# Kernel optimization log

Hardware: AMD Instinct MI355X
Metric: run time of the kernel (lower is better)

Reference implementation:

```python
import jax, jax.numpy as jnp
import numpy as np
from jax import lax

SINKHORN_ITERS = 20


def sinkhorn_knopp(logits, tau=1.0, iterations=SINKHORN_ITERS):
    # logits: [N, K]. Log-domain alternating row/col normalization.
    N, K = logits.shape
    P = logits / tau
    log_target_col_sum = jnp.log(jnp.asarray(N / K, dtype=logits.dtype) + 1e-9)

    def step(P, _):
        P = P - jax.nn.logsumexp(P, axis=1, keepdims=True)   # row sums -> 1
        P = P - jax.nn.logsumexp(P, axis=0, keepdims=True) + log_target_col_sum  # col sums -> N/K
        return P, None

    P, _ = lax.scan(step, P, None, length=iterations)
    return jnp.exp(P)


def setup_inputs() -> dict:
    key = jax.random.key(0)
    ks = jax.random.split(key, 8)
    N, C, K, B = 200000, 128, 32, 16
    x = jax.random.normal(ks[0], (N, C), dtype=jnp.float32)
    batch = jnp.sort(jax.random.randint(ks[1], (N,), 0, B))
    # assign_mlp: Linear(C,C) -> ReLU -> Linear(C,K)
    W1 = jax.random.normal(ks[2], (C, C), dtype=jnp.float32) / np.sqrt(C)
    b1 = jnp.zeros((C,), dtype=jnp.float32)
    W2 = jax.random.normal(ks[3], (C, K), dtype=jnp.float32) / np.sqrt(C)
    b2 = jnp.zeros((K,), dtype=jnp.float32)
    scaling = jnp.asarray(5.0, dtype=jnp.float32)
    return {"x": x, "batch": batch, "W1": W1, "b1": b1, "W2": W2, "b2": b2,
            "scaling": scaling, "num_graphs": B}


def reference(x, batch, W1, b1, W2, b2, scaling, num_graphs):
    # assignment logits: MLP(x) * scaling  -> [N, K]
    h = jax.nn.relu(x @ W1 + b1)
    logits = (h @ W2 + b2) * scaling
    # doubly-stochastic soft assignment via Sinkhorn-Knopp (tau=1.0, 20 iters)
    s = sinkhorn_knopp(logits, tau=1.0, iterations=SINKHORN_ITERS)  # [N, K]
    # pooled super-node features: scatter-sum over graphs of s[n,k]*x[n,c]
    onehot = jax.nn.one_hot(batch, num_graphs, dtype=x.dtype)        # [N, B]
    out = jnp.einsum('nb,nk,nc->bkc', onehot, s, x)                  # [B, K, C]
    return out
```

## Files before the change

### kernel.cpp

```cpp
#include <hip/hip_runtime.h>
#include <hip/hip_bf16.h>

#define C_DIM 128
#define K_DIM 32
#define N_ITERS 20
#define NSHARD 16
#define WPAD 136
#define SK_THREADS 832
#define SK_WAVES 13

typedef __attribute__((ext_vector_type(8))) short short8;
typedef __attribute__((ext_vector_type(4))) float f32x4;
typedef __attribute__((ext_vector_type(4))) unsigned short us4;

__device__ __forceinline__ unsigned short f2bf(float f) {
    __hip_bfloat16 h = __float2bfloat16(f);
    return *reinterpret_cast<unsigned short*>(&h);
}

__global__ void init_kernel(float* __restrict__ out, int n_out,
                            float* __restrict__ zreg, int n_z,
                            const float* __restrict__ W1, const float* __restrict__ W2,
                            unsigned short* __restrict__ W1t,
                            unsigned short* __restrict__ W2t) {
    int i = blockIdx.x * blockDim.x + threadIdx.x;
    int stride = gridDim.x * blockDim.x;
    for (int j = i; j < n_out; j += stride) out[j] = 0.f;
    for (int j = i; j < n_z; j += stride) zreg[j] = 0.f;
    for (int j = i; j < C_DIM * C_DIM; j += stride) {
        int n = j >> 7, k = j & 127;
        W1t[j] = f2bf(W1[k * C_DIM + n]);
    }
    for (int j = i; j < C_DIM * K_DIM; j += stride) {
        int n = j >> 7, k = j & 127;
        W2t[j] = f2bf(W2[k * K_DIM + n]);
    }
}

__global__ __launch_bounds__(256, 4) void mlp_kernel(
    const float* __restrict__ x, const unsigned short* __restrict__ W1t,
    const float* __restrict__ b1, const unsigned short* __restrict__ W2t,
    const float* __restrict__ b2, const float* __restrict__ scal,
    float* __restrict__ Lg, int N, int ntiles) {
    __shared__ unsigned short sW1[C_DIM][WPAD];
    __shared__ unsigned short sW2[K_DIM][WPAD];
    __shared__ unsigned short sX[64][WPAD];
    __shared__ unsigned short sH[4][16][WPAD];
    __shared__ float sB1[C_DIM];
    __shared__ float sB2[K_DIM];

    const int tid = threadIdx.x;
    for (int i = tid; i < C_DIM * 16; i += 256) {
        const int r = i >> 4, c8 = (i & 15) * 8;
        *(float4*)&sW1[r][c8] = *(const float4*)&W1t[r * C_DIM + c8];
    }
    for (int i = tid; i < K_DIM * 16; i += 256) {
        const int r = i >> 4, c8 = (i & 15) * 8;
        *(float4*)&sW2[r][c8] = *(const float4*)&W2t[r * C_DIM + c8];
    }
    if (tid < C_DIM) sB1[tid] = b1[tid];
    if (tid < K_DIM) sB2[tid] = b2[tid];
    const float sc = *scal;

    const int wave = tid >> 6;
    const int lane = tid & 63;
    const int lr = lane & 15;
    const int kg = lane >> 4;
    __syncthreads();

    for (int tile = blockIdx.x; tile < ntiles; tile += gridDim.x) {
        const int row0 = tile * 64;
        __syncthreads();
        for (int i = tid; i < 2048; i += 256) {
            const int r = i >> 5, c4 = (i & 31) * 4;
            const float4 v = *(const float4*)&x[(size_t)(row0 + r) * C_DIM + c4];
            us4 u;
            u.x = f2bf(v.x); u.y = f2bf(v.y); u.z = f2bf(v.z); u.w = f2bf(v.w);
            *(us4*)&sX[r][c4] = u;
        }
        __syncthreads();

        short8 a[4];
#pragma unroll
        for (int kt = 0; kt < 4; ++kt)
            a[kt] = *(const short8*)&sX[wave * 16 + lr][kt * 32 + kg * 8];
#pragma unroll
        for (int ct = 0; ct < 8; ++ct) {
            const float bv = sB1[ct * 16 + lr];
            f32x4 acc = {bv, bv, bv, bv};
#pragma unroll
            for (int kt = 0; kt < 4; ++kt) {
                const short8 b = *(const short8*)&sW1[ct * 16 + lr][kt * 32 + kg * 8];
                acc = __builtin_amdgcn_mfma_f32_16x16x32_bf16(a[kt], b, acc, 0, 0, 0);
            }
#pragma unroll
            for (int r = 0; r < 4; ++r)
                sH[wave][kg * 4 + r][ct * 16 + lr] = f2bf(fmaxf(acc[r], 0.f));
        }
        __syncthreads();

        short8 a2[4];
#pragma unroll
        for (int kt = 0; kt < 4; ++kt)
            a2[kt] = *(const short8*)&sH[wave][lr][kt * 32 + kg * 8];
#pragma unroll
        for (int ct = 0; ct < 2; ++ct) {
            const float bv = sB2[ct * 16 + lr];
            f32x4 acc = {bv, bv, bv, bv};
#pragma unroll
            for (int kt = 0; kt < 4; ++kt) {
                const short8 b = *(const short8*)&sW2[ct * 16 + lr][kt * 32 + kg * 8];
                acc = __builtin_amdgcn_mfma_f32_16x16x32_bf16(a2[kt], b, acc, 0, 0, 0);
            }
#pragma unroll
            for (int r = 0; r < 4; ++r) {
                const int g = row0 + wave * 16 + kg * 4 + r;
                Lg[(size_t)g * K_DIM + ct * 16 + lr] = acc[r] * sc;
            }
        }
    }
}

__device__ __forceinline__ int bitrev5(int l) {
    return ((l & 1) << 4) | ((l & 2) << 2) | (l & 4) | ((l & 8) >> 2) |
           ((l & 16) >> 4);
}

#define FOLD_STAGE(M, HALF)                                   \
    {                                                         \
        const bool hi = (lane & (M)) != 0;                    \
        _Pragma("unroll")                                     \
        for (int j = 0; j < (HALF); ++j) {                    \
            const float give = hi ? p[j] : p[j + (HALF)];     \
            const float keep = hi ? p[j + (HALF)] : p[j];     \
            p[j] = keep + __shfl_xor(give, (M));              \
        }                                                     \
    }

__global__ __launch_bounds__(SK_THREADS) void sinkhorn_kernel(
    float* __restrict__ Lg, float* __restrict__ shards,
    float* __restrict__ vglob, int* __restrict__ arrive, int* __restrict__ done,
    int N, int nblocks) {
    __shared__ float sv[K_DIM];
    __shared__ float swsum[SK_WAVES][K_DIM];
    __shared__ float sdl[K_DIM];
    __shared__ int is_last;
    const int tid = threadIdx.x;
    const int wave = tid >> 6;
    const int lane = tid & 63;
    const size_t n = (size_t)blockIdx.x * SK_THREADS + tid;
    const bool valid = n < (size_t)N;
    const int myshard = blockIdx.x & (NSHARD - 1);
    const float log_tgt = __logf((float)N / (float)K_DIM);

    if (tid < K_DIM) sv[tid] = 0.f;

    float L[K_DIM];
    if (valid) {
        const float4* Lr = (const float4*)(Lg + n * K_DIM);
#pragma unroll
        for (int j = 0; j < 8; ++j) {
            const float4 v = Lr[j];
            L[4 * j] = v.x; L[4 * j + 1] = v.y; L[4 * j + 2] = v.z; L[4 * j + 3] = v.w;
        }
    } else {
#pragma unroll
        for (int j = 0; j < K_DIM; ++j) L[j] = 0.f;
    }
    __syncthreads();

    float m0 = 0.f, inv = 0.f;
    for (int t = 1; t <= N_ITERS; ++t) {
        float p[K_DIM];
        if (valid) {
#pragma unroll
            for (int j = 0; j < K_DIM; ++j) p[j] = L[j] - sv[j];
            m0 = p[0];
#pragma unroll
            for (int j = 1; j < K_DIM; ++j) m0 = fmaxf(m0, p[j]);
            float sum = 0.f;
#pragma unroll
            for (int j = 0; j < K_DIM; ++j) {
                p[j] = __expf(p[j] - m0);
                sum += p[j];
            }
            inv = 1.f / sum;
#pragma unroll
            for (int j = 0; j < K_DIM; ++j) p[j] *= inv;
        } else {
#pragma unroll
            for (int j = 0; j < K_DIM; ++j) p[j] = 0.f;
        }

        FOLD_STAGE(1, 16)
        FOLD_STAGE(2, 8)
        FOLD_STAGE(4, 4)
        FOLD_STAGE(8, 2)
        FOLD_STAGE(16, 1)
        const float tot = p[0] + __shfl_xor(p[0], 32);
        if (lane < K_DIM) swsum[wave][bitrev5(lane)] = tot;
        __syncthreads();
        if (tid < K_DIM) {
            float s_ = 0.f;
#pragma unroll
            for (int w = 0; w < SK_WAVES; ++w) s_ += swsum[w][tid];
            atomicAdd(&shards[((size_t)t * NSHARD + myshard) * K_DIM + tid], s_);
        }
        asm volatile("s_waitcnt vmcnt(0)" ::: "memory");
        __syncthreads();
        if (tid == 0) {
            const int old = __hip_atomic_fetch_add(arrive + t, 1, __ATOMIC_RELAXED,
                                                   __HIP_MEMORY_SCOPE_AGENT);
            is_last = (old == nblocks - 1);
        }
        __syncthreads();
        if (is_last) {
            if (tid < K_DIM) {
                float cs = 0.f;
#pragma unroll
                for (int sh = 0; sh < NSHARD; ++sh)
                    cs += __hip_atomic_load(
                        &shards[((size_t)t * NSHARD + sh) * K_DIM + tid],
                        __ATOMIC_RELAXED, __HIP_MEMORY_SCOPE_AGENT);
                const float v = (t < N_ITERS) ? (__logf(cs) - log_tgt)
                                              : ((float)N / (float)K_DIM) / cs;
                __hip_atomic_store(&vglob[t * K_DIM + tid], v, __ATOMIC_RELAXED,
                                   __HIP_MEMORY_SCOPE_AGENT);
            }
            asm volatile("s_waitcnt vmcnt(0)" ::: "memory");
            __syncthreads();
            if (tid == 0)
                __hip_atomic_store(done + t, 1, __ATOMIC_RELAXED,
                                   __HIP_MEMORY_SCOPE_AGENT);
        } else {
            if (tid == 0) {
                while (__hip_atomic_load(done + t, __ATOMIC_RELAXED,
                                         __HIP_MEMORY_SCOPE_AGENT) == 0)
                    __builtin_amdgcn_s_sleep(2);
            }
        }
        __syncthreads();
        if (tid < K_DIM) {
            const float v = __hip_atomic_load(&vglob[t * K_DIM + tid],
                                              __ATOMIC_RELAXED,
                                              __HIP_MEMORY_SCOPE_AGENT);
            if (t < N_ITERS) sv[tid] += v;
            else sdl[tid] = v;
        }
        __syncthreads();
    }

    if (valid) {
        float4* Sr = (float4*)(Lg + n * K_DIM);
#pragma unroll
        for (int j = 0; j < 8; ++j) {
            float4 o;
            o.x = __expf(L[4 * j + 0] - sv[4 * j + 0] - m0) * inv * sdl[4 * j + 0];
            o.y = __expf(L[4 * j + 1] - sv[4 * j + 1] - m0) * inv * sdl[4 * j + 1];
            o.z = __expf(L[4 * j + 2] - sv[4 * j + 2] - m0) * inv * sdl[4 * j + 2];
            o.w = __expf(L[4 * j + 3] - sv[4 * j + 3] - m0) * inv * sdl[4 * j + 3];
            Sr[j] = o;
        }
    }
}

#define PCHUNK 96
#define PCH_PER_BLOCK 4

__global__ __launch_bounds__(256) void pool_kernel(
    const float* __restrict__ x, const int* __restrict__ batch,
    const float* __restrict__ Sg, float* __restrict__ out, int N) {
    __shared__ float sx[PCHUNK][C_DIM];
    __shared__ float ss[PCHUNK][K_DIM];
    __shared__ int sb[PCHUNK];

    const int tid = threadIdx.x;
    const int k0 = (tid >> 5) * 4;
    const int c0 = (tid & 31) * 4;
    float acc[4][4];
#pragma unroll
    for (int i = 0; i < 4; ++i)
#pragma unroll
        for (int j = 0; j < 4; ++j) acc[i][j] = 0.f;

    int cur_b = -1;
    const int base0 = blockIdx.x * (PCHUNK * PCH_PER_BLOCK);

    for (int cc = 0; cc < PCH_PER_BLOCK; ++cc) {
        const int base = base0 + cc * PCHUNK;
        if (base >= N) break;
        const int rows = min(PCHUNK, N - base);
        __syncthreads();
        {
            const float4* src = (const float4*)(x + (size_t)base * C_DIM);
            for (int i = tid; i < rows * (C_DIM / 4); i += 256)
                ((float4*)&sx[0][0])[i] = src[i];
            const float4* ssrc = (const float4*)(Sg + (size_t)base * K_DIM);
            for (int i = tid; i < rows * (K_DIM / 4); i += 256)
                ((float4*)&ss[0][0])[i] = ssrc[i];
        }
        if (tid < rows) sb[tid] = batch[base + tid];
        __syncthreads();

        for (int r = 0; r < rows; ++r) {
            const int b = sb[r];
            if (b != cur_b) {
                if (cur_b >= 0) {
                    float* ob = out + ((size_t)cur_b * K_DIM + k0) * C_DIM + c0;
#pragma unroll
                    for (int i = 0; i < 4; ++i)
#pragma unroll
                        for (int j = 0; j < 4; ++j) {
                            atomicAdd(&ob[i * C_DIM + j], acc[i][j]);
                            acc[i][j] = 0.f;
                        }
                }
                cur_b = b;
            }
            const float4 sv = *(const float4*)&ss[r][k0];
            const float4 xv = *(const float4*)&sx[r][c0];
            const float sA[4] = {sv.x, sv.y, sv.z, sv.w};
            const float xA[4] = {xv.x, xv.y, xv.z, xv.w};
#pragma unroll
            for (int i = 0; i < 4; ++i)
#pragma unroll
                for (int j = 0; j < 4; ++j)
                    acc[i][j] = fmaf(sA[i], xA[j], acc[i][j]);
        }
    }
    if (cur_b >= 0) {
        float* ob = out + ((size_t)cur_b * K_DIM + k0) * C_DIM + c0;
#pragma unroll
        for (int i = 0; i < 4; ++i)
#pragma unroll
            for (int j = 0; j < 4; ++j) atomicAdd(&ob[i * C_DIM + j], acc[i][j]);
    }
}

extern "C" void kernel_launch(void* const* d_in, const int* in_sizes, int n_in,
                              void* d_out, int out_size, void* d_ws, size_t ws_size,
                              hipStream_t stream) {
    const float* x = (const float*)d_in[0];
    const int* batch = (const int*)d_in[1];
    const float* W1 = (const float*)d_in[2];
    const float* b1 = (const float*)d_in[3];
    const float* W2 = (const float*)d_in[4];
    const float* b2 = (const float*)d_in[5];
    const float* scal = (const float*)d_in[6];
    float* out = (float*)d_out;

    const int N = in_sizes[1];

    float* Lg = (float*)d_ws;
    float* shards = Lg + (size_t)N * K_DIM;
    const int n_shard_f = (N_ITERS + 1) * NSHARD * K_DIM;
    int* arrive = (int*)(shards + n_shard_f);
    int* done = arrive + 32;
    float* vglob = (float*)(done + 32);
    const int n_vglob = (N_ITERS + 1) * K_DIM;
    unsigned short* W1t = (unsigned short*)(vglob + n_vglob);
    unsigned short* W2t = W1t + C_DIM * C_DIM;
    const int n_z = n_shard_f + 64 + n_vglob;

    init_kernel<<<64, 256, 0, stream>>>(out, out_size, shards, n_z,
                                        W1, W2, W1t, W2t);

    const int ntiles = N / 64;
    mlp_kernel<<<640, 256, 0, stream>>>(x, W1t, b1, W2t, b2, scal, Lg, N, ntiles);

    const int sblocks = 256;
    sinkhorn_kernel<<<sblocks, SK_THREADS, 0, stream>>>(Lg, shards, vglob,
                                                        arrive, done, N, sblocks);

    const int pblocks = (N + PCHUNK * PCH_PER_BLOCK - 1) / (PCHUNK * PCH_PER_BLOCK);
    pool_kernel<<<pblocks, 256, 0, stream>>>(x, batch, Lg, out, N);
}
```

Before: 491.1 us.

## Precompute exp of logits and use hierarchical grid barrier in Sinkhorn

The Sinkhorn loop is rewritten in the multiplicative domain. Each row's exp(L - max) is computed once, so every iteration reduces to a dot product with per-column scale factors and one reciprocal, replacing 32 exps per row per iteration. The single-level grid barrier, where all blocks atomically arrive on one counter and spin on one flag, becomes a two-level tree: 16 groups of 16 blocks, with group leaders signalling followers. This should cut both ALU work and barrier contention, but it adds more flags and spin paths, and the multiplicative form can overflow or underflow when column scales grow large.

```diff
diff --git a/kernel.cpp b/kernel.cpp
--- a/kernel.cpp
+++ b/kernel.cpp
@@ -4,10 +4,11 @@
 #define C_DIM 128
 #define K_DIM 32
 #define N_ITERS 20
-#define NSHARD 16
 #define WPAD 136
 #define SK_THREADS 832
 #define SK_WAVES 13
+#define NGRP 16
+#define GSIZE 16
 
 typedef __attribute__((ext_vector_type(8))) short short8;
 typedef __attribute__((ext_vector_type(4))) float f32x4;
@@ -138,59 +139,53 @@
     }
 
 __global__ __launch_bounds__(SK_THREADS) void sinkhorn_kernel(
-    float* __restrict__ Lg, float* __restrict__ shards,
-    float* __restrict__ vglob, int* __restrict__ arrive, int* __restrict__ done,
-    int N, int nblocks) {
+    float* __restrict__ Lg, float* __restrict__ shards, float* __restrict__ vglob,
+    int* __restrict__ garr, int* __restrict__ rarr, int* __restrict__ done,
+    int* __restrict__ gdone, int N) {
     __shared__ float sv[K_DIM];
+    __shared__ float sw[K_DIM];
+    __shared__ float swsd[K_DIM];
     __shared__ float swsum[SK_WAVES][K_DIM];
-    __shared__ float sdl[K_DIM];
-    __shared__ int is_last;
     const int tid = threadIdx.x;
     const int wave = tid >> 6;
     const int lane = tid & 63;
+    const int g = blockIdx.x >> 4;
     const size_t n = (size_t)blockIdx.x * SK_THREADS + tid;
     const bool valid = n < (size_t)N;
-    const int myshard = blockIdx.x & (NSHARD - 1);
     const float log_tgt = __logf((float)N / (float)K_DIM);
 
-    if (tid < K_DIM) sv[tid] = 0.f;
-
-    float L[K_DIM];
+    if (tid < K_DIM) { sv[tid] = 0.f; sw[tid] = 1.f; }
+
+    float E[K_DIM];
     if (valid) {
         const float4* Lr = (const float4*)(Lg + n * K_DIM);
 #pragma unroll
         for (int j = 0; j < 8; ++j) {
             const float4 v = Lr[j];
-            L[4 * j] = v.x; L[4 * j + 1] = v.y; L[4 * j + 2] = v.z; L[4 * j + 3] = v.w;
-        }
+            E[4 * j] = v.x; E[4 * j + 1] = v.y; E[4 * j + 2] = v.z; E[4 * j + 3] = v.w;
+        }
+        float M = E[0];
+#pragma unroll
+        for (int j = 1; j < K_DIM; ++j) M = fmaxf(M, E[j]);
+#pragma unroll
+        for (int j = 0; j < K_DIM; ++j) E[j] = __expf(E[j] - M);
     } else {
 #pragma unroll
-        for (int j = 0; j < K_DIM; ++j) L[j] = 0.f;
+        for (int j = 0; j < K_DIM; ++j) E[j] = 0.f;
     }
     __syncthreads();
 
-    float m0 = 0.f, inv = 0.f;
+    float r_last = 0.f;
     for (int t = 1; t <= N_ITERS; ++t) {
+        float up = 0.f;
+#pragma unroll
+        for (int j = 0; j < K_DIM; ++j) up = fmaf(E[j], sw[j], up);
+        float r = 0.f;
+        if (valid) r = 1.0f / up;
+        r_last = r;
         float p[K_DIM];
-        if (valid) {
-#pragma unroll
-            for (int j = 0; j < K_DIM; ++j) p[j] = L[j] - sv[j];
-            m0 = p[0];
-#pragma unroll
-            for (int j = 1; j < K_DIM; ++j) m0 = fmaxf(m0, p[j]);
-            float sum = 0.f;
-#pragma unroll
-            for (int j = 0; j < K_DIM; ++j) {
-                p[j] = __expf(p[j] - m0);
-                sum += p[j];
-            }
-            inv = 1.f / sum;
-#pragma unroll
-            for (int j = 0; j < K_DIM; ++j) p[j] *= inv;
-        } else {
-#pragma unroll
-            for (int j = 0; j < K_DIM; ++j) p[j] = 0.f;
-        }
+#pragma unroll
+        for (int j = 0; j < K_DIM; ++j) p[j] = E[j] * r;
 
         FOLD_STAGE(1, 16)
         FOLD_STAGE(2, 8)
@@ -200,52 +195,77 @@
         const float tot = p[0] + __shfl_xor(p[0], 32);
         if (lane < K_DIM) swsum[wave][bitrev5(lane)] = tot;
         __syncthreads();
-        if (tid < K_DIM) {
-            float s_ = 0.f;
-#pragma unroll
-            for (int w = 0; w < SK_WAVES; ++w) s_ += swsum[w][tid];
-            atomicAdd(&shards[((size_t)t * NSHARD + myshard) * K_DIM + tid], s_);
-        }
-        asm volatile("s_waitcnt vmcnt(0)" ::: "memory");
-        __syncthreads();
-        if (tid == 0) {
-            const int old = __hip_atomic_fetch_add(arrive + t, 1, __ATOMIC_RELAXED,
-                                                   __HIP_MEMORY_SCOPE_AGENT);
-            is_last = (old == nblocks - 1);
-        }
-        __syncthreads();
-        if (is_last) {
-            if (tid < K_DIM) {
-                float cs = 0.f;
-#pragma unroll
-                for (int sh = 0; sh < NSHARD; ++sh)
-                    cs += __hip_atomic_load(
-                        &shards[((size_t)t * NSHARD + sh) * K_DIM + tid],
-                        __ATOMIC_RELAXED, __HIP_MEMORY_SCOPE_AGENT);
-                const float v = (t < N_ITERS) ? (__logf(cs) - log_tgt)
-                                              : ((float)N / (float)K_DIM) / cs;
-                __hip_atomic_store(&vglob[t * K_DIM + tid], v, __ATOMIC_RELAXED,
-                                   __HIP_MEMORY_SCOPE_AGENT);
+
+        if (wave == 0) {
+            if (lane < K_DIM) {
+                float s_ = 0.f;
+#pragma unroll
+                for (int w = 0; w < SK_WAVES; ++w) s_ += swsum[w][lane];
+                atomicAdd(&shards[((size_t)t * NGRP + g) * K_DIM + lane], s_);
             }
             asm volatile("s_waitcnt vmcnt(0)" ::: "memory");
-            __syncthreads();
-            if (tid == 0)
-                __hip_atomic_store(done + t, 1, __ATOMIC_RELAXED,
-                                   __HIP_MEMORY_SCOPE_AGENT);
-        } else {
-            if (tid == 0) {
-                while (__hip_atomic_load(done + t, __ATOMIC_RELAXED,
-                                         __HIP_MEMORY_SCOPE_AGENT) == 0)
-                    __builtin_amdgcn_s_sleep(2);
-            }
-        }
-        __syncthreads();
-        if (tid < K_DIM) {
-            const float v = __hip_atomic_load(&vglob[t * K_DIM + tid],
-                                              __ATOMIC_RELAXED,
-                                              __HIP_MEMORY_SCOPE_AGENT);
-            if (t < N_ITERS) sv[tid] += v;
-            else sdl[tid] = v;
+            int is_gl = 0, is_rl = 0;
+            if (lane == 0) {
+                const int ga = __hip_atomic_fetch_add(&garr[t * NGRP + g], 1,
+                                                      __ATOMIC_RELAXED,
+                                                      __HIP_MEMORY_SCOPE_AGENT);
+                is_gl = (ga == GSIZE - 1);
+                if (is_gl) {
+                    const int ra = __hip_atomic_fetch_add(&rarr[t], 1,
+                                                          __ATOMIC_RELAXED,
+                                                          __HIP_MEMORY_SCOPE_AGENT);
+                    is_rl = (ra == NGRP - 1);
+                }
+            }
+            is_gl = __shfl(is_gl, 0);
+            is_rl = __shfl(is_rl, 0);
+            if (is_rl) {
+                if (lane < K_DIM) {
+                    float cs = 0.f;
+#pragma unroll
+                    for (int gg = 0; gg < NGRP; ++gg)
+                        cs += __hip_atomic_load(
+                            &shards[((size_t)t * NGRP + gg) * K_DIM + lane],
+                            __ATOMIC_RELAXED, __HIP_MEMORY_SCOPE_AGENT);
+                    cs *= sw[lane];
+                    const float v = (t < N_ITERS) ? (__logf(cs) - log_tgt)
+                                                  : ((float)N / (float)K_DIM) / cs;
+                    __hip_atomic_store(&vglob[t * K_DIM + lane], v,
+                                       __ATOMIC_RELAXED, __HIP_MEMORY_SCOPE_AGENT);
+                }
+                asm volatile("s_waitcnt vmcnt(0)" ::: "memory");
+                if (lane == 0) {
+                    __hip_atomic_store(done + t, 1, __ATOMIC_RELAXED,
+                                       __HIP_MEMORY_SCOPE_AGENT);
+                    __hip_atomic_store(&gdone[t * NGRP + g], 1, __ATOMIC_RELAXED,
+                                       __HIP_MEMORY_SCOPE_AGENT);
+                }
+            } else if (is_gl) {
+                if (lane == 0) {
+                    while (__hip_atomic_load(done + t, __ATOMIC_RELAXED,
+                                             __HIP_MEMORY_SCOPE_AGENT) == 0)
+                        __builtin_amdgcn_s_sleep(1);
+                    __hip_atomic_store(&gdone[t * NGRP + g], 1, __ATOMIC_RELAXED,
+                                       __HIP_MEMORY_SCOPE_AGENT);
+                }
+            } else {
+                if (lane == 0) {
+                    while (__hip_atomic_load(&gdone[t * NGRP + g], __ATOMIC_RELAXED,
+                                             __HIP_MEMORY_SCOPE_AGENT) == 0)
+                        __builtin_amdgcn_s_sleep(1);
+                }
+            }
+            if (lane < K_DIM) {
+                const float v = __hip_atomic_load(&vglob[t * K_DIM + lane],
+                                                  __ATOMIC_RELAXED,
+                                                  __HIP_MEMORY_SCOPE_AGENT);
+                if (t < N_ITERS) {
+                    sv[lane] += v;
+                    sw[lane] = __expf(-sv[lane]);
+                } else {
+                    swsd[lane] = sw[lane] * v;
+                }
+            }
         }
         __syncthreads();
     }
@@ -255,10 +275,10 @@
 #pragma unroll
         for (int j = 0; j < 8; ++j) {
             float4 o;
-            o.x = __expf(L[4 * j + 0] - sv[4 * j + 0] - m0) * inv * sdl[4 * j + 0];
-            o.y = __expf(L[4 * j + 1] - sv[4 * j + 1] - m0) * inv * sdl[4 * j + 1];
-            o.z = __expf(L[4 * j + 2] - sv[4 * j + 2] - m0) * inv * sdl[4 * j + 2];
-            o.w = __expf(L[4 * j + 3] - sv[4 * j + 3] - m0) * inv * sdl[4 * j + 3];
+            o.x = E[4 * j + 0] * swsd[4 * j + 0] * r_last;
+            o.y = E[4 * j + 1] * swsd[4 * j + 1] * r_last;
+            o.z = E[4 * j + 2] * swsd[4 * j + 2] * r_last;
+            o.w = E[4 * j + 3] * swsd[4 * j + 3] * r_last;
             Sr[j] = o;
         }
     }
@@ -353,14 +373,16 @@
 
     float* Lg = (float*)d_ws;
     float* shards = Lg + (size_t)N * K_DIM;
-    const int n_shard_f = (N_ITERS + 1) * NSHARD * K_DIM;
-    int* arrive = (int*)(shards + n_shard_f);
-    int* done = arrive + 32;
-    float* vglob = (float*)(done + 32);
+    const int n_shard_f = (N_ITERS + 1) * NGRP * K_DIM;
+    float* vglob = shards + n_shard_f;
     const int n_vglob = (N_ITERS + 1) * K_DIM;
-    unsigned short* W1t = (unsigned short*)(vglob + n_vglob);
+    int* garr = (int*)(vglob + n_vglob);
+    int* rarr = garr + 352;
+    int* done = rarr + 32;
+    int* gdone = done + 32;
+    unsigned short* W1t = (unsigned short*)(gdone + 352);
     unsigned short* W2t = W1t + C_DIM * C_DIM;
-    const int n_z = n_shard_f + 64 + n_vglob;
+    const int n_z = n_shard_f + n_vglob + 352 + 32 + 32 + 352;
 
     init_kernel<<<64, 256, 0, stream>>>(out, out_size, shards, n_z,
                                         W1, W2, W1t, W2t);
@@ -368,9 +390,9 @@
     const int ntiles = N / 64;
     mlp_kernel<<<640, 256, 0, stream>>>(x, W1t, b1, W2t, b2, scal, Lg, N, ntiles);
 
-    const int sblocks = 256;
+    const int sblocks = NGRP * GSIZE;
     sinkhorn_kernel<<<sblocks, SK_THREADS, 0, stream>>>(Lg, shards, vglob,
-                                                        arrive, done, N, sblocks);
+                                                        garr, rarr, done, gdone, N);
 
     const int pblocks = (N + PCHUNK * PCH_PER_BLOCK - 1) / (PCHUNK * PCH_PER_BLOCK);
     pool_kernel<<<pblocks, 256, 0, stream>>>(x, batch, Lg, out, N);
```

After: 496.9 us. Within noise of the previous version (+1.2%).
